# Kernel optimization log

Measured on AMD Instinct MI355X. Metric: run time of the kernel, lower is better.

## Reference

```python
import jax, jax.numpy as jnp
import numpy as np

N_NODES = 100_000
N_EDGES = 1_600_000
F_IN = 64
HID = 128
HEAD_H = 256
OUT = 32
N_GRAPHS = 512
NEG_SLOPE = 0.01  # torch.nn.LeakyReLU default


def _leaky(v):
    return jnp.where(v >= 0, v, NEG_SLOPE * v)


def _gine_layer(x, src, dst, edge_attr, We, be, Wn, bn, n_nodes):
    # GINEConv (eps=0): nn( x_i + sum_j relu(x_j + lin(edge_attr_ji)) )
    msg = jax.nn.relu(x[src] + edge_attr @ We + be)          # [E, in]
    agg = jax.ops.segment_sum(msg, dst, num_segments=n_nodes)  # [N, in]
    return (agg + x) @ Wn + bn                                # [N, hid]


def setup_inputs() -> dict:
    key = jax.random.key(0)
    ks = jax.random.split(key, 24)
    inp = {}
    inp["x"] = jax.random.normal(ks[0], (N_NODES, F_IN), dtype=jnp.float32)
    inp["edge_index"] = jax.random.randint(ks[1], (2, N_EDGES), 0, N_NODES, dtype=jnp.int32)
    inp["edge_attr"] = jax.random.normal(ks[2], (N_EDGES, 2), dtype=jnp.float32)
    inp["batch"] = jnp.sort(jax.random.randint(ks[3], (N_NODES,), 0, N_GRAPHS, dtype=jnp.int32))
    # GINE layers: edge lin (2 -> in) and nn Linear (in -> hid)
    dims = [F_IN, HID, HID]
    ki = 4
    for l, d_in in enumerate(dims):
        inp[f"We{l}"] = jax.random.normal(ks[ki], (2, d_in), dtype=jnp.float32) / np.sqrt(2.0); ki += 1
        inp[f"be{l}"] = jnp.zeros((d_in,), dtype=jnp.float32)
        inp[f"Wn{l}"] = jax.random.normal(ks[ki], (d_in, HID), dtype=jnp.float32) / np.sqrt(d_in); ki += 1
        inp[f"bn{l}"] = jnp.zeros((HID,), dtype=jnp.float32)
    # head MLP
    inp["Wh0"] = jax.random.normal(ks[ki], (HID, HEAD_H), dtype=jnp.float32) / np.sqrt(HID); ki += 1
    inp["bh0"] = jnp.zeros((HEAD_H,), dtype=jnp.float32)
    inp["Wh1"] = jax.random.normal(ks[ki], (HEAD_H, OUT), dtype=jnp.float32) / np.sqrt(HEAD_H); ki += 1
    inp["bh1"] = jnp.zeros((OUT,), dtype=jnp.float32)
    return inp


def reference(x, edge_index, edge_attr, batch,
              We0, be0, Wn0, bn0,
              We1, be1, Wn1, bn1,
              We2, be2, Wn2, bn2,
              Wh0, bh0, Wh1, bh1):
    src, dst = edge_index[0], edge_index[1]
    h = _leaky(_gine_layer(x, src, dst, edge_attr, We0, be0, Wn0, bn0, N_NODES))
    h = _leaky(_gine_layer(h, src, dst, edge_attr, We1, be1, Wn1, bn1, N_NODES))
    h = _leaky(_gine_layer(h, src, dst, edge_attr, We2, be2, Wn2, bn2, N_NODES))
    pooled = jax.ops.segment_sum(h, batch, num_segments=N_GRAPHS)  # [G, HID]
    h = _leaky(pooled @ Wh0 + bh0)
    return h @ Wh1 + bh1  # [G, OUT]
```

## Files before the change

### kernel.cpp

```cpp
#include <hip/hip_runtime.h>
#include <hip/hip_bf16.h>

#define N_NODES 100000
#define N_EDGES 1600000
#define F_IN 64
#define HID 128
#define HEAD_H 256
#define OUT_F 32
#define N_GRAPHS 512
#define NBK 98
#define BCHUNK 4096
#define NCHUNKS ((N_EDGES + BCHUNK - 1) / BCHUNK)

typedef float f2v __attribute__((ext_vector_type(2)));
typedef short bf16x8 __attribute__((ext_vector_type(8)));
typedef float f32x4 __attribute__((ext_vector_type(4)));

__device__ __forceinline__ float leaky(float v) {
    return v >= 0.f ? v : 0.01f * v;
}

__device__ __forceinline__ float bf2f(ushort u) {
    union { uint i; float f; } c; c.i = ((uint)u) << 16; return c.f;
}

__device__ __forceinline__ ushort f2bf(float f) {
    union { float f; uint i; } c; c.f = f;
    uint r = c.i + 0x7FFF + ((c.i >> 16) & 1);
    return (ushort)(r >> 16);
}

__global__ __launch_bounds__(256) void cast_kernel(const float* __restrict__ x,
                                                   ushort* __restrict__ xb, int n2) {
    int i = blockIdx.x * 256 + threadIdx.x;
    if (i < n2) {
        float2 v = ((const float2*)x)[i];
        uint u = (uint)f2bf(v.x) | ((uint)f2bf(v.y) << 16);
        ((uint*)xb)[i] = u;
    }
}

__global__ __launch_bounds__(256) void prep_wnT(const float* __restrict__ Wn0,
                                                const float* __restrict__ Wn1,
                                                const float* __restrict__ Wn2,
                                                ushort* __restrict__ w0T,
                                                ushort* __restrict__ w1T,
                                                ushort* __restrict__ w2T) {
    int id = blockIdx.x * 256 + threadIdx.x;
    if (id < 128 * 64) {
        int j = id / 64, k = id % 64;
        w0T[id] = f2bf(Wn0[k * 128 + j]);
    } else if (id < 128 * 64 + 128 * 128) {
        int t = id - 128 * 64; int j = t / 128, k = t % 128;
        w1T[t] = f2bf(Wn1[k * 128 + j]);
    } else if (id < 128 * 64 + 2 * 128 * 128) {
        int t = id - 128 * 64 - 128 * 128; int j = t / 128, k = t % 128;
        w2T[t] = f2bf(Wn2[k * 128 + j]);
    }
}


__global__ __launch_bounds__(256) void bucket_hist(const int* __restrict__ dst,
                                                   int* __restrict__ cnt98) {
    __shared__ int h[NBK];
    int tid = threadIdx.x;
    if (tid < NBK) h[tid] = 0;
    __syncthreads();
    int e0 = blockIdx.x * BCHUNK;
    int nn = N_EDGES - e0; if (nn > BCHUNK) nn = BCHUNK;
    for (int i = tid; i < nn; i += 256) {
        atomicAdd(&h[dst[e0 + i] >> 10], 1);
    }
    __syncthreads();
    if (tid < NBK && h[tid] > 0) atomicAdd(&cnt98[tid], h[tid]);
}

__global__ __launch_bounds__(128) void bucket_scan(const int* __restrict__ cnt98,
                                                   int* __restrict__ bbase,
                                                   int* __restrict__ bcur,
                                                   int* __restrict__ rowptr) {
    __shared__ int sd[128];
    int t = threadIdx.x;
    int v = (t < NBK) ? cnt98[t] : 0;
    sd[t] = v;
    __syncthreads();
    for (int off = 1; off < 128; off <<= 1) {
        int u = (t >= off) ? sd[t - off] : 0;
        __syncthreads();
        sd[t] += u;
        __syncthreads();
    }
    if (t < NBK) {
        int ex = sd[t] - v;
        bbase[t] = ex;
        bcur[t] = ex;
    }
    if (t == 0) {
        bbase[NBK] = N_EDGES;
        rowptr[N_NODES] = N_EDGES;
    }
}

__global__ __launch_bounds__(256) void bin_kernel(const int* __restrict__ src,
                                                  const int* __restrict__ dst,
                                                  const float2* __restrict__ ea,
                                                  int* __restrict__ bcur,
                                                  uint2* __restrict__ recs1) {
    __shared__ int hist[NBK], tmp[NBK], offs[NBK], cur[NBK], gbase[NBK];
    __shared__ uint2 stage[BCHUNK];
    __shared__ unsigned char sbid[BCHUNK];

    int tid = threadIdx.x;
    int e0 = blockIdx.x * BCHUNK;
    int nn = N_EDGES - e0; if (nn > BCHUNK) nn = BCHUNK;

    if (tid < NBK) hist[tid] = 0;
    __syncthreads();

    for (int i = tid; i < nn; i += 256) {
        atomicAdd(&hist[dst[e0 + i] >> 10], 1);
    }
    __syncthreads();

    if (tid < NBK) tmp[tid] = hist[tid];
    __syncthreads();
    for (int off = 1; off < NBK; off <<= 1) {
        int u = (tid < NBK && tid >= off) ? tmp[tid - off] : 0;
        __syncthreads();
        if (tid < NBK) tmp[tid] += u;
        __syncthreads();
    }
    if (tid < NBK) {
        int ex = tmp[tid] - hist[tid];
        offs[tid] = ex;
        cur[tid] = ex;
        gbase[tid] = (hist[tid] > 0) ? atomicAdd(&bcur[tid], hist[tid]) : 0;
    }
    __syncthreads();

    for (int i = tid; i < nn; i += 256) {
        int e = e0 + i;
        int d = dst[e];
        int b = d >> 10;
        int dloc = d & 1023;
        float2 a = ea[e];
        uint2 r;
        r.x = (uint)src[e] | ((uint)dloc << 22);
        r.y = (uint)f2bf(a.x) | ((uint)f2bf(a.y) << 16);
        int pos = atomicAdd(&cur[b], 1);
        stage[pos] = r;
        sbid[pos] = (unsigned char)b;
    }
    __syncthreads();

    for (int i = tid; i < nn; i += 256) {
        int b = sbid[i];
        recs1[gbase[b] + (i - offs[b])] = stage[i];
    }
}

__global__ __launch_bounds__(256) void order_kernel(const uint2* __restrict__ recs1,
                                                    const int* __restrict__ bbase,
                                                    int* __restrict__ rowptr,
                                                    uint2* __restrict__ recs2) {
    __shared__ int h[1024];
    __shared__ int ssum[256];
    int b = blockIdx.x;
    int tid = threadIdx.x;
    int base = bbase[b];
    int end = bbase[b + 1];

    for (int i = tid; i < 1024; i += 256) h[i] = 0;
    __syncthreads();

    for (int t = base + tid; t < end; t += 256) {
        atomicAdd(&h[recs1[t].x >> 22], 1);
    }
    __syncthreads();

    int i4 = tid * 4;
    int a0 = h[i4], a1 = h[i4 + 1], a2 = h[i4 + 2], a3 = h[i4 + 3];
    int s = a0 + a1 + a2 + a3;
    ssum[tid] = s;
    __syncthreads();
    for (int off = 1; off < 256; off <<= 1) {
        int u = (tid >= off) ? ssum[tid - off] : 0;
        __syncthreads();
        ssum[tid] += u;
        __syncthreads();
    }
    int pre = base + ssum[tid] - s;
    int c0 = pre, c1 = pre + a0, c2 = c1 + a1, c3 = c2 + a2;
    h[i4] = c0; h[i4 + 1] = c1; h[i4 + 2] = c2; h[i4 + 3] = c3;

    int n = (b << 10) + i4;
    if (n + 4 <= N_NODES) {
        *(int4*)(rowptr + n) = make_int4(c0, c1, c2, c3);
    } else {
        if (n + 0 < N_NODES) rowptr[n + 0] = c0;
        if (n + 1 < N_NODES) rowptr[n + 1] = c1;
        if (n + 2 < N_NODES) rowptr[n + 2] = c2;
        if (n + 3 < N_NODES) rowptr[n + 3] = c3;
    }
    __syncthreads();

    for (int t = base + tid; t < end; t += 256) {
        uint2 r = recs1[t];
        int pos = atomicAdd(&h[r.x >> 22], 1);
        recs2[pos] = make_uint2(r.x & 0x3FFFFFu, r.y);
    }
}


template <int D>
__global__ __launch_bounds__(256) void gine_gather(const ushort* __restrict__ xb,
                                                   const uint2* __restrict__ recs,
                                                   const int* __restrict__ rowptr,
                                                   const float* __restrict__ We,
                                                   const float* __restrict__ be,
                                                   ushort* __restrict__ tb) {
    int node = (blockIdx.x * 256 + (int)threadIdx.x) >> 6;
    int lane = threadIdx.x & 63;
    if (node >= N_NODES) return;

    int rs = __builtin_amdgcn_readfirstlane(rowptr[node]);
    int re = __builtin_amdgcn_readfirstlane(rowptr[node + 1]);

    if constexpr (D == 128) {
        int j = lane * 2;
        f2v w0v = {We[j], We[j + 1]};
        f2v w1v = {We[128 + j], We[128 + j + 1]};
        f2v bbv = {be[j], be[j + 1]};
        f2v accv = {0.f, 0.f};
        const f2v zero = {0.f, 0.f};

        auto proc = [&](uint2 r, uint u) {
            float ax = bf2f((ushort)(r.y & 0xFFFF));
            float ay = bf2f((ushort)(r.y >> 16));
            union { uint i; float f; } lo, hi;
            lo.i = u << 16;
            hi.i = u & 0xFFFF0000u;
            f2v xv = {lo.f, hi.f};
            f2v m = xv + bbv;
            m = ay * w1v + m;
            m = ax * w0v + m;
            m = __builtin_elementwise_max(m, zero);
            accv += m;
        };

        int t = rs;
        for (; t + 7 < re; t += 8) {
            uint2 r0 = recs[t];
            uint2 r1 = recs[t + 1];
            uint2 r2 = recs[t + 2];
            uint2 r3 = recs[t + 3];
            uint2 r4 = recs[t + 4];
            uint2 r5 = recs[t + 5];
            uint2 r6 = recs[t + 6];
            uint2 r7 = recs[t + 7];
            uint u0 = *(const uint*)(xb + (size_t)r0.x * 128 + j);
            uint u1 = *(const uint*)(xb + (size_t)r1.x * 128 + j);
            uint u2 = *(const uint*)(xb + (size_t)r2.x * 128 + j);
            uint u3 = *(const uint*)(xb + (size_t)r3.x * 128 + j);
            uint u4 = *(const uint*)(xb + (size_t)r4.x * 128 + j);
            uint u5 = *(const uint*)(xb + (size_t)r5.x * 128 + j);
            uint u6 = *(const uint*)(xb + (size_t)r6.x * 128 + j);
            uint u7 = *(const uint*)(xb + (size_t)r7.x * 128 + j);
            proc(r0, u0); proc(r1, u1); proc(r2, u2); proc(r3, u3);
            proc(r4, u4); proc(r5, u5); proc(r6, u6); proc(r7, u7);
        }
        for (; t + 3 < re; t += 4) {
            uint2 r0 = recs[t];
            uint2 r1 = recs[t + 1];
            uint2 r2 = recs[t + 2];
            uint2 r3 = recs[t + 3];
            uint u0 = *(const uint*)(xb + (size_t)r0.x * 128 + j);
            uint u1 = *(const uint*)(xb + (size_t)r1.x * 128 + j);
            uint u2 = *(const uint*)(xb + (size_t)r2.x * 128 + j);
            uint u3 = *(const uint*)(xb + (size_t)r3.x * 128 + j);
            proc(r0, u0); proc(r1, u1); proc(r2, u2); proc(r3, u3);
        }
        for (; t < re; t++) {
            uint2 r0 = recs[t];
            uint u0 = *(const uint*)(xb + (size_t)r0.x * 128 + j);
            proc(r0, u0);
        }

        {
            uint u = *(const uint*)(xb + (size_t)node * 128 + j);
            union { uint i; float f; } lo, hi;
            lo.i = u << 16;
            hi.i = u & 0xFFFF0000u;
            f2v xv = {lo.f, hi.f};
            accv += xv;
        }
        uint up = (uint)f2bf(accv.x) | ((uint)f2bf(accv.y) << 16);
        ((uint*)tb)[(size_t)node * 64 + lane] = up;
    } else {
        float w0 = We[lane], w1 = We[64 + lane], bb = be[lane];
        float acc = 0.f;

        auto proc = [&](uint2 r, ushort u) {
            float ax = bf2f((ushort)(r.y & 0xFFFF));
            float ay = bf2f((ushort)(r.y >> 16));
            float m = bf2f(u) + bb;
            m = ay * w1 + m;
            m = ax * w0 + m;
            acc += fmaxf(m, 0.f);
        };

        int t = rs;
        for (; t + 7 < re; t += 8) {
            uint2 r0 = recs[t];
            uint2 r1 = recs[t + 1];
            uint2 r2 = recs[t + 2];
            uint2 r3 = recs[t + 3];
            uint2 r4 = recs[t + 4];
            uint2 r5 = recs[t + 5];
            uint2 r6 = recs[t + 6];
            uint2 r7 = recs[t + 7];
            ushort u0 = xb[(size_t)r0.x * 64 + lane];
            ushort u1 = xb[(size_t)r1.x * 64 + lane];
            ushort u2 = xb[(size_t)r2.x * 64 + lane];
            ushort u3 = xb[(size_t)r3.x * 64 + lane];
            ushort u4 = xb[(size_t)r4.x * 64 + lane];
            ushort u5 = xb[(size_t)r5.x * 64 + lane];
            ushort u6 = xb[(size_t)r6.x * 64 + lane];
            ushort u7 = xb[(size_t)r7.x * 64 + lane];
            proc(r0, u0); proc(r1, u1); proc(r2, u2); proc(r3, u3);
            proc(r4, u4); proc(r5, u5); proc(r6, u6); proc(r7, u7);
        }
        for (; t + 3 < re; t += 4) {
            uint2 r0 = recs[t];
            uint2 r1 = recs[t + 1];
            uint2 r2 = recs[t + 2];
            uint2 r3 = recs[t + 3];
            ushort u0 = xb[(size_t)r0.x * 64 + lane];
            ushort u1 = xb[(size_t)r1.x * 64 + lane];
            ushort u2 = xb[(size_t)r2.x * 64 + lane];
            ushort u3 = xb[(size_t)r3.x * 64 + lane];
            proc(r0, u0); proc(r1, u1); proc(r2, u2); proc(r3, u3);
        }
        for (; t < re; t++) {
            uint2 r0 = recs[t];
            ushort u0 = xb[(size_t)r0.x * 64 + lane];
            proc(r0, u0);
        }
        acc += bf2f(xb[(size_t)node * 64 + lane]);
        tb[(size_t)node * 64 + lane] = f2bf(acc);
    }
}


template <int K>
__global__ __launch_bounds__(256) void gine_transform_mfma(const ushort* __restrict__ tb,
                                                           const ushort* __restrict__ wnT,
                                                           const float* __restrict__ bn,
                                                           ushort* __restrict__ hb) {
    int wave = threadIdx.x >> 6;
    int lane = threadIdx.x & 63;
    int m0 = blockIdx.x * 64 + wave * 16;
    int l15 = lane & 15;
    int kgrp = (lane >> 4) * 8;

    const ushort* aptr = tb + (size_t)(m0 + l15) * K + kgrp;

    f32x4 acc[8];
#pragma unroll
    for (int nt = 0; nt < 8; nt++) {
        float b = bn[nt * 16 + l15];
        acc[nt] = {b, b, b, b};
    }

#pragma unroll
    for (int kk = 0; kk < K / 32; kk++) {
        bf16x8 a = *(const bf16x8*)(aptr + kk * 32);
#pragma unroll
        for (int nt = 0; nt < 8; nt++) {
            bf16x8 bfrag = *(const bf16x8*)(wnT + (size_t)(nt * 16 + l15) * K + kk * 32 + kgrp);
            acc[nt] = __builtin_amdgcn_mfma_f32_16x16x32_bf16(a, bfrag, acc[nt], 0, 0, 0);
        }
    }

    int rbase = m0 + (lane >> 4) * 4;
#pragma unroll
    for (int nt = 0; nt < 8; nt++) {
#pragma unroll
        for (int r = 0; r < 4; r++) {
            int nd = rbase + r;
            if (nd < N_NODES)
                hb[(size_t)nd * HID + nt * 16 + l15] = f2bf(leaky(acc[nt][r]));
        }
    }
}

#define POOL_NPW 64
__global__ __launch_bounds__(256) void pool_kernel(const ushort* __restrict__ h,
                                                   const int* __restrict__ batch,
                                                   float* __restrict__ pooled) {
    int wid = (blockIdx.x * 256 + (int)threadIdx.x) >> 6;
    int lane = threadIdx.x & 63;
    int n0 = wid * POOL_NPW;
    if (n0 >= N_NODES) return;
    int n1 = n0 + POOL_NPW; if (n1 > N_NODES) n1 = N_NODES;

    int j = lane * 2;
    f2v acc = {0.f, 0.f};
    int g = __builtin_amdgcn_readfirstlane(batch[n0]);
    for (int i = n0; i < n1; i++) {
        int bg = __builtin_amdgcn_readfirstlane(batch[i]);
        if (bg != g) {
            atomicAdd(&pooled[g * HID + j], acc.x);
            atomicAdd(&pooled[g * HID + j + 1], acc.y);
            acc.x = 0.f; acc.y = 0.f;
            g = bg;
        }
        uint u = *(const uint*)(h + (size_t)i * HID + j);
        union { uint i; float f; } lo, hi;
        lo.i = u << 16;
        hi.i = u & 0xFFFF0000u;
        acc.x += lo.f;
        acc.y += hi.f;
    }
    atomicAdd(&pooled[g * HID + j], acc.x);
    atomicAdd(&pooled[g * HID + j + 1], acc.y);
}


__global__ __launch_bounds__(256) void head_kernel(const float* __restrict__ pooled,
                                                   const float* __restrict__ Wh0,
                                                   const float* __restrict__ bh0,
                                                   const float* __restrict__ Wh1,
                                                   const float* __restrict__ bh1,
                                                   float* __restrict__ out) {
    __shared__ float p[HID];
    __shared__ float hid[HEAD_H];
    int g = blockIdx.x;
    int t = threadIdx.x;
    if (t < HID) p[t] = pooled[g * HID + t];
    __syncthreads();
    float acc = bh0[t];
    for (int k = 0; k < HID; k++) acc += p[k] * Wh0[k * HEAD_H + t];
    hid[t] = leaky(acc);
    __syncthreads();
    if (t < OUT_F) {
        float o = bh1[t];
        for (int k = 0; k < HEAD_H; k++) o += hid[k] * Wh1[k * OUT_F + t];
        out[g * OUT_F + t] = o;
    }
}

extern "C" void kernel_launch(void* const* d_in, const int* in_sizes, int n_in,
                              void* d_out, int out_size, void* d_ws, size_t ws_size,
                              hipStream_t stream) {
    const float* x     = (const float*)d_in[0];
    const int*   ei    = (const int*)d_in[1];
    const float* ea    = (const float*)d_in[2];
    const int*   batch = (const int*)d_in[3];
    const float* We0 = (const float*)d_in[4];
    const float* be0 = (const float*)d_in[5];
    const float* Wn0 = (const float*)d_in[6];
    const float* bn0 = (const float*)d_in[7];
    const float* We1 = (const float*)d_in[8];
    const float* be1 = (const float*)d_in[9];
    const float* Wn1 = (const float*)d_in[10];
    const float* bn1 = (const float*)d_in[11];
    const float* We2 = (const float*)d_in[12];
    const float* be2 = (const float*)d_in[13];
    const float* Wn2 = (const float*)d_in[14];
    const float* bn2 = (const float*)d_in[15];
    const float* Wh0 = (const float*)d_in[16];
    const float* bh0 = (const float*)d_in[17];
    const float* Wh1 = (const float*)d_in[18];
    const float* bh1 = (const float*)d_in[19];

    const int* src = ei;
    const int* dst = ei + N_EDGES;

    char* ws = (char*)d_ws;
    size_t o = 0;
    uint2*  recs1 = (uint2*)(ws + o); o += (size_t)N_EDGES * 8;
    uint2*  recs2 = (uint2*)(ws + o); o += (size_t)N_EDGES * 8;
    ushort* xb0  = (ushort*)(ws + o); o += (size_t)N_NODES * 64 * 2;
    ushort* tbuf = (ushort*)(ws + o); o += (size_t)N_NODES * 128 * 2;
    ushort* hbuf = (ushort*)(ws + o); o += (size_t)N_NODES * 128 * 2;
    int*    rowptr = (int*)(ws + o);  o += 400128;
    int*    cnt98  = (int*)(ws + o);  o += 4096;
    int*    bbase  = (int*)(ws + o);  o += 4096;
    int*    bcur   = (int*)(ws + o);  o += 4096;
    ushort* wnT0 = (ushort*)(ws + o); o += 128 * 64 * 2;
    ushort* wnT1 = (ushort*)(ws + o); o += 128 * 128 * 2;
    ushort* wnT2 = (ushort*)(ws + o); o += 128 * 128 * 2;
    float*  pooled = (float*)(ws + o); o += (size_t)N_GRAPHS * HID * 4;

    cast_kernel<<<(N_NODES * F_IN / 2 + 255) / 256, 256, 0, stream>>>(x, xb0, N_NODES * F_IN / 2);
    prep_wnT<<<160, 256, 0, stream>>>(Wn0, Wn1, Wn2, wnT0, wnT1, wnT2);

    hipMemsetAsync(cnt98, 0, NBK * sizeof(int), stream);
    bucket_hist<<<NCHUNKS, 256, 0, stream>>>(dst, cnt98);
    bucket_scan<<<1, 128, 0, stream>>>(cnt98, bbase, bcur, rowptr);
    bin_kernel<<<NCHUNKS, 256, 0, stream>>>(src, dst, (const float2*)ea, bcur, recs1);
    order_kernel<<<NBK, 256, 0, stream>>>(recs1, bbase, rowptr, recs2);

    const int GATHER_BLOCKS = (N_NODES * 64 + 255) / 256;
    const int TRANS_BLOCKS  = (N_NODES + 63) / 64;

    gine_gather<64><<<GATHER_BLOCKS, 256, 0, stream>>>(xb0, recs2, rowptr, We0, be0, tbuf);
    gine_transform_mfma<64><<<TRANS_BLOCKS, 256, 0, stream>>>(tbuf, wnT0, bn0, hbuf);

    gine_gather<128><<<GATHER_BLOCKS, 256, 0, stream>>>(hbuf, recs2, rowptr, We1, be1, tbuf);
    gine_transform_mfma<128><<<TRANS_BLOCKS, 256, 0, stream>>>(tbuf, wnT1, bn1, hbuf);

    gine_gather<128><<<GATHER_BLOCKS, 256, 0, stream>>>(hbuf, recs2, rowptr, We2, be2, tbuf);
    gine_transform_mfma<128><<<TRANS_BLOCKS, 256, 0, stream>>>(tbuf, wnT2, bn2, hbuf);

    hipMemsetAsync(pooled, 0, (size_t)N_GRAPHS * HID * sizeof(float), stream);
    pool_kernel<<<(N_NODES / POOL_NPW + 3) / 4, 256, 0, stream>>>(hbuf, batch, pooled);
    head_kernel<<<N_GRAPHS, 256, 0, stream>>>(pooled, Wh0, bh0, Wh1, bh1, (float*)d_out);
}
```

Baseline: 393.8 us.

## Fuse edge gather and MFMA node transform into one kernel per GINE layer

Replaces the separate gather and MFMA transform kernels with one fused kernel per layer. Each 1024-thread block handles 16 nodes: its 16 waves split the block's edge range evenly and accumulate into swizzled LDS with shared-memory atomics. The first 8 waves then add the self features and run the 16x16x32 bf16 MFMA straight from LDS. This removes the bf16 intermediate buffer round trip and two launches, and evens out per-wave edge load. In exchange it adds LDS atomic traffic, block-wide barriers, and only half the waves working in the matmul phase.

```diff
diff --git a/kernel.cpp b/kernel.cpp
--- a/kernel.cpp
+++ b/kernel.cpp
@@ -207,34 +207,58 @@
     for (int t = base + tid; t < end; t += 256) {
         uint2 r = recs1[t];
         int pos = atomicAdd(&h[r.x >> 22], 1);
-        recs2[pos] = make_uint2(r.x & 0x3FFFFFu, r.y);
-    }
-}
-
-
-template <int D>
-__global__ __launch_bounds__(256) void gine_gather(const ushort* __restrict__ xb,
+        recs2[pos] = r;
+    }
+}
+
+
+template <int K>
+__global__ __launch_bounds__(1024) void gine_fused(const ushort* __restrict__ xb,
                                                    const uint2* __restrict__ recs,
                                                    const int* __restrict__ rowptr,
                                                    const float* __restrict__ We,
                                                    const float* __restrict__ be,
-                                                   ushort* __restrict__ tb) {
-    int node = (blockIdx.x * 256 + (int)threadIdx.x) >> 6;
-    int lane = threadIdx.x & 63;
-    if (node >= N_NODES) return;
-
-    int rs = __builtin_amdgcn_readfirstlane(rowptr[node]);
-    int re = __builtin_amdgcn_readfirstlane(rowptr[node + 1]);
-
-    if constexpr (D == 128) {
+                                                   const ushort* __restrict__ wnT,
+                                                   const float* __restrict__ bn,
+                                                   ushort* __restrict__ hb) {
+    __shared__ float acc_s[16 * K];
+    int tid = threadIdx.x;
+    int wave = __builtin_amdgcn_readfirstlane(tid >> 6);
+    int lane = tid & 63;
+    int n0 = blockIdx.x * 16;
+
+    for (int i = tid; i < 16 * K; i += 1024) acc_s[i] = 0.f;
+
+    int base = __builtin_amdgcn_readfirstlane(rowptr[n0]);
+    int end  = __builtin_amdgcn_readfirstlane(rowptr[n0 + 16]);
+    __syncthreads();
+
+    int E = end - base;
+    int per = (E + 15) >> 4;
+    int t0 = base + wave * per;
+    int t1 = t0 + per; if (t1 > end) t1 = end;
+
+    if constexpr (K == 128) {
         int j = lane * 2;
         f2v w0v = {We[j], We[j + 1]};
         f2v w1v = {We[128 + j], We[128 + j + 1]};
         f2v bbv = {be[j], be[j + 1]};
         f2v accv = {0.f, 0.f};
         const f2v zero = {0.f, 0.f};
-
+        int cur = -1;
+
+        auto flush = [&]() {
+            int idx = (cur * 128 + j) ^ ((cur & 7) << 2);
+            atomicAdd(&acc_s[idx], accv.x);
+            atomicAdd(&acc_s[idx + 1], accv.y);
+        };
         auto proc = [&](uint2 r, uint u) {
+            int local = (int)(r.x >> 22) & 15;
+            if (local != cur) {
+                if (cur >= 0) flush();
+                cur = local;
+                accv = zero;
+            }
             float ax = bf2f((ushort)(r.y & 0xFFFF));
             float ay = bf2f((ushort)(r.y >> 16));
             union { uint i; float f; } lo, hi;
@@ -248,59 +272,40 @@
             accv += m;
         };
 
-        int t = rs;
-        for (; t + 7 < re; t += 8) {
+        int t = t0;
+        for (; t + 3 < t1; t += 4) {
             uint2 r0 = recs[t];
             uint2 r1 = recs[t + 1];
             uint2 r2 = recs[t + 2];
             uint2 r3 = recs[t + 3];
-            uint2 r4 = recs[t + 4];
-            uint2 r5 = recs[t + 5];
-            uint2 r6 = recs[t + 6];
-            uint2 r7 = recs[t + 7];
-            uint u0 = *(const uint*)(xb + (size_t)r0.x * 128 + j);
-            uint u1 = *(const uint*)(xb + (size_t)r1.x * 128 + j);
-            uint u2 = *(const uint*)(xb + (size_t)r2.x * 128 + j);
-            uint u3 = *(const uint*)(xb + (size_t)r3.x * 128 + j);
-            uint u4 = *(const uint*)(xb + (size_t)r4.x * 128 + j);
-            uint u5 = *(const uint*)(xb + (size_t)r5.x * 128 + j);
-            uint u6 = *(const uint*)(xb + (size_t)r6.x * 128 + j);
-            uint u7 = *(const uint*)(xb + (size_t)r7.x * 128 + j);
+            uint u0 = *(const uint*)(xb + (size_t)(r0.x & 0x3FFFFFu) * 128 + j);
+            uint u1 = *(const uint*)(xb + (size_t)(r1.x & 0x3FFFFFu) * 128 + j);
+            uint u2 = *(const uint*)(xb + (size_t)(r2.x & 0x3FFFFFu) * 128 + j);
+            uint u3 = *(const uint*)(xb + (size_t)(r3.x & 0x3FFFFFu) * 128 + j);
             proc(r0, u0); proc(r1, u1); proc(r2, u2); proc(r3, u3);
-            proc(r4, u4); proc(r5, u5); proc(r6, u6); proc(r7, u7);
-        }
-        for (; t + 3 < re; t += 4) {
+        }
+        for (; t < t1; t++) {
             uint2 r0 = recs[t];
-            uint2 r1 = recs[t + 1];
-            uint2 r2 = recs[t + 2];
-            uint2 r3 = recs[t + 3];
-            uint u0 = *(const uint*)(xb + (size_t)r0.x * 128 + j);
-            uint u1 = *(const uint*)(xb + (size_t)r1.x * 128 + j);
-            uint u2 = *(const uint*)(xb + (size_t)r2.x * 128 + j);
-            uint u3 = *(const uint*)(xb + (size_t)r3.x * 128 + j);
-            proc(r0, u0); proc(r1, u1); proc(r2, u2); proc(r3, u3);
-        }
-        for (; t < re; t++) {
-            uint2 r0 = recs[t];
-            uint u0 = *(const uint*)(xb + (size_t)r0.x * 128 + j);
+            uint u0 = *(const uint*)(xb + (size_t)(r0.x & 0x3FFFFFu) * 128 + j);
             proc(r0, u0);
         }
-
-        {
-            uint u = *(const uint*)(xb + (size_t)node * 128 + j);
-            union { uint i; float f; } lo, hi;
-            lo.i = u << 16;
-            hi.i = u & 0xFFFF0000u;
-            f2v xv = {lo.f, hi.f};
-            accv += xv;
-        }
-        uint up = (uint)f2bf(accv.x) | ((uint)f2bf(accv.y) << 16);
-        ((uint*)tb)[(size_t)node * 64 + lane] = up;
+        if (cur >= 0) flush();
     } else {
         float w0 = We[lane], w1 = We[64 + lane], bb = be[lane];
         float acc = 0.f;
-
+        int cur = -1;
+
+        auto flush = [&]() {
+            int idx = (cur * 64 + lane) ^ ((cur & 7) << 2);
+            atomicAdd(&acc_s[idx], acc);
+        };
         auto proc = [&](uint2 r, ushort u) {
+            int local = (int)(r.x >> 22) & 15;
+            if (local != cur) {
+                if (cur >= 0) flush();
+                cur = local;
+                acc = 0.f;
+            }
             float ax = bf2f((ushort)(r.y & 0xFFFF));
             float ay = bf2f((ushort)(r.y >> 16));
             float m = bf2f(u) + bb;
@@ -309,87 +314,58 @@
             acc += fmaxf(m, 0.f);
         };
 
-        int t = rs;
-        for (; t + 7 < re; t += 8) {
+        int t = t0;
+        for (; t + 3 < t1; t += 4) {
             uint2 r0 = recs[t];
             uint2 r1 = recs[t + 1];
             uint2 r2 = recs[t + 2];
             uint2 r3 = recs[t + 3];
-            uint2 r4 = recs[t + 4];
-            uint2 r5 = recs[t + 5];
-            uint2 r6 = recs[t + 6];
-            uint2 r7 = recs[t + 7];
-            ushort u0 = xb[(size_t)r0.x * 64 + lane];
-            ushort u1 = xb[(size_t)r1.x * 64 + lane];
-            ushort u2 = xb[(size_t)r2.x * 64 + lane];
-            ushort u3 = xb[(size_t)r3.x * 64 + lane];
-            ushort u4 = xb[(size_t)r4.x * 64 + lane];
-            ushort u5 = xb[(size_t)r5.x * 64 + lane];
-            ushort u6 = xb[(size_t)r6.x * 64 + lane];
-            ushort u7 = xb[(size_t)r7.x * 64 + lane];
+            ushort u0 = xb[(size_t)(r0.x & 0x3FFFFFu) * 64 + lane];
+            ushort u1 = xb[(size_t)(r1.x & 0x3FFFFFu) * 64 + lane];
+            ushort u2 = xb[(size_t)(r2.x & 0x3FFFFFu) * 64 + lane];
+            ushort u3 = xb[(size_t)(r3.x & 0x3FFFFFu) * 64 + lane];
             proc(r0, u0); proc(r1, u1); proc(r2, u2); proc(r3, u3);
-            proc(r4, u4); proc(r5, u5); proc(r6, u6); proc(r7, u7);
-        }
-        for (; t + 3 < re; t += 4) {
+        }
+        for (; t < t1; t++) {
             uint2 r0 = recs[t];
-            uint2 r1 = recs[t + 1];
-            uint2 r2 = recs[t + 2];
-            uint2 r3 = recs[t + 3];
-            ushort u0 = xb[(size_t)r0.x * 64 + lane];
-            ushort u1 = xb[(size_t)r1.x * 64 + lane];
-            ushort u2 = xb[(size_t)r2.x * 64 + lane];
-            ushort u3 = xb[(size_t)r3.x * 64 + lane];
-            proc(r0, u0); proc(r1, u1); proc(r2, u2); proc(r3, u3);
-        }
-        for (; t < re; t++) {
-            uint2 r0 = recs[t];
-            ushort u0 = xb[(size_t)r0.x * 64 + lane];
+            ushort u0 = xb[(size_t)(r0.x & 0x3FFFFFu) * 64 + lane];
             proc(r0, u0);
         }
-        acc += bf2f(xb[(size_t)node * 64 + lane]);
-        tb[(size_t)node * 64 + lane] = f2bf(acc);
-    }
-}
-
-
-template <int K>
-__global__ __launch_bounds__(256) void gine_transform_mfma(const ushort* __restrict__ tb,
-                                                           const ushort* __restrict__ wnT,
-                                                           const float* __restrict__ bn,
-                                                           ushort* __restrict__ hb) {
-    int wave = threadIdx.x >> 6;
-    int lane = threadIdx.x & 63;
-    int m0 = blockIdx.x * 64 + wave * 16;
-    int l15 = lane & 15;
-    int kgrp = (lane >> 4) * 8;
-
-    const ushort* aptr = tb + (size_t)(m0 + l15) * K + kgrp;
-
-    f32x4 acc[8];
+        if (cur >= 0) flush();
+    }
+    __syncthreads();
+
+    if (wave < 8) {
+        int nt = wave;
+        int l15 = lane & 15;
+        int kgrp = (lane >> 4) * 8;
+        int row = l15;
+        int sw = (row & 7) << 2;
+        float b = bn[nt * 16 + l15];
+        f32x4 acc = {b, b, b, b};
+
 #pragma unroll
-    for (int nt = 0; nt < 8; nt++) {
-        float b = bn[nt * 16 + l15];
-        acc[nt] = {b, b, b, b};
-    }
-
+        for (int kk = 0; kk < K / 32; kk++) {
+            int k0 = kk * 32 + kgrp;
+            int i0 = (row * K + k0) ^ sw;
+            int i1 = (row * K + k0 + 4) ^ sw;
+            f32x4 p0 = *(const f32x4*)&acc_s[i0];
+            f32x4 p1 = *(const f32x4*)&acc_s[i1];
+            bf16x8 xr = *(const bf16x8*)(xb + (size_t)(n0 + row) * K + k0);
+            bf16x8 a;
 #pragma unroll
-    for (int kk = 0; kk < K / 32; kk++) {
-        bf16x8 a = *(const bf16x8*)(aptr + kk * 32);
-#pragma unroll
-        for (int nt = 0; nt < 8; nt++) {
-            bf16x8 bfrag = *(const bf16x8*)(wnT + (size_t)(nt * 16 + l15) * K + kk * 32 + kgrp);
-            acc[nt] = __builtin_amdgcn_mfma_f32_16x16x32_bf16(a, bfrag, acc[nt], 0, 0, 0);
-        }
-    }
-
-    int rbase = m0 + (lane >> 4) * 4;
-#pragma unroll
-    for (int nt = 0; nt < 8; nt++) {
+            for (int e = 0; e < 4; e++) {
+                a[e]     = (short)f2bf(p0[e] + bf2f((ushort)xr[e]));
+                a[e + 4] = (short)f2bf(p1[e] + bf2f((ushort)xr[e + 4]));
+            }
+            bf16x8 bfrag = *(const bf16x8*)(wnT + (size_t)(nt * 16 + l15) * K + k0);
+            acc = __builtin_amdgcn_mfma_f32_16x16x32_bf16(a, bfrag, acc, 0, 0, 0);
+        }
+
+        int rbase = n0 + (lane >> 4) * 4;
 #pragma unroll
         for (int r = 0; r < 4; r++) {
-            int nd = rbase + r;
-            if (nd < N_NODES)
-                hb[(size_t)nd * HID + nt * 16 + l15] = f2bf(leaky(acc[nt][r]));
+            hb[(size_t)(rbase + r) * HID + nt * 16 + l15] = f2bf(leaky(acc[r]));
         }
     }
 }
@@ -482,8 +458,8 @@
     uint2*  recs1 = (uint2*)(ws + o); o += (size_t)N_EDGES * 8;
     uint2*  recs2 = (uint2*)(ws + o); o += (size_t)N_EDGES * 8;
     ushort* xb0  = (ushort*)(ws + o); o += (size_t)N_NODES * 64 * 2;
-    ushort* tbuf = (ushort*)(ws + o); o += (size_t)N_NODES * 128 * 2;
-    ushort* hbuf = (ushort*)(ws + o); o += (size_t)N_NODES * 128 * 2;
+    ushort* hbufA = (ushort*)(ws + o); o += (size_t)N_NODES * 128 * 2;
+    ushort* hbufB = (ushort*)(ws + o); o += (size_t)N_NODES * 128 * 2;
     int*    rowptr = (int*)(ws + o);  o += 400128;
     int*    cnt98  = (int*)(ws + o);  o += 4096;
     int*    bbase  = (int*)(ws + o);  o += 4096;
@@ -502,19 +478,13 @@
     bin_kernel<<<NCHUNKS, 256, 0, stream>>>(src, dst, (const float2*)ea, bcur, recs1);
     order_kernel<<<NBK, 256, 0, stream>>>(recs1, bbase, rowptr, recs2);
 
-    const int GATHER_BLOCKS = (N_NODES * 64 + 255) / 256;
-    const int TRANS_BLOCKS  = (N_NODES + 63) / 64;
-
-    gine_gather<64><<<GATHER_BLOCKS, 256, 0, stream>>>(xb0, recs2, rowptr, We0, be0, tbuf);
-    gine_transform_mfma<64><<<TRANS_BLOCKS, 256, 0, stream>>>(tbuf, wnT0, bn0, hbuf);
-
-    gine_gather<128><<<GATHER_BLOCKS, 256, 0, stream>>>(hbuf, recs2, rowptr, We1, be1, tbuf);
-    gine_transform_mfma<128><<<TRANS_BLOCKS, 256, 0, stream>>>(tbuf, wnT1, bn1, hbuf);
-
-    gine_gather<128><<<GATHER_BLOCKS, 256, 0, stream>>>(hbuf, recs2, rowptr, We2, be2, tbuf);
-    gine_transform_mfma<128><<<TRANS_BLOCKS, 256, 0, stream>>>(tbuf, wnT2, bn2, hbuf);
+    const int FUSED_BLOCKS = N_NODES / 16;
+
+    gine_fused<64><<<FUSED_BLOCKS, 1024, 0, stream>>>(xb0, recs2, rowptr, We0, be0, wnT0, bn0, hbufA);
+    gine_fused<128><<<FUSED_BLOCKS, 1024, 0, stream>>>(hbufA, recs2, rowptr, We1, be1, wnT1, bn1, hbufB);
+    gine_fused<128><<<FUSED_BLOCKS, 1024, 0, stream>>>(hbufB, recs2, rowptr, We2, be2, wnT2, bn2, hbufA);
 
     hipMemsetAsync(pooled, 0, (size_t)N_GRAPHS * HID * sizeof(float), stream);
-    pool_kernel<<<(N_NODES / POOL_NPW + 3) / 4, 256, 0, stream>>>(hbuf, batch, pooled);
+    pool_kernel<<<(N_NODES / POOL_NPW + 3) / 4, 256, 0, stream>>>(hbufA, batch, pooled);
     head_kernel<<<N_GRAPHS, 256, 0, stream>>>(pooled, Wh0, bh0, Wh1, bh1, (float*)d_out);
 }
```

Result: slower. 570.5 us (+44.9%).

## Fuse GINE gather and MFMA transform into one kernel per layer

Applied to the files above, without the earlier changes.

Merges the per-layer edge gather-aggregate and the bf16 MFMA node transform into a single kernel. Each block of four waves aggregates 16 nodes into a swizzled fp32 LDS tile, adds the self features, then runs the 16x128 MFMA with each wave computing two output column tiles. This drops the intermediate tbuf round trip and one launch per layer, and ping-pongs between two h buffers. In exchange each block covers only 16 rows, so the Wn fragments are reloaded from global/L2 per block, and each wave walks four nodes in sequence, which can increase load imbalance.

```diff
diff --git a/kernel.cpp b/kernel.cpp
--- a/kernel.cpp
+++ b/kernel.cpp
@@ -212,184 +212,188 @@
 }
 
 
-template <int D>
-__global__ __launch_bounds__(256) void gine_gather(const ushort* __restrict__ xb,
-                                                   const uint2* __restrict__ recs,
-                                                   const int* __restrict__ rowptr,
-                                                   const float* __restrict__ We,
-                                                   const float* __restrict__ be,
-                                                   ushort* __restrict__ tb) {
-    int node = (blockIdx.x * 256 + (int)threadIdx.x) >> 6;
-    int lane = threadIdx.x & 63;
-    if (node >= N_NODES) return;
-
-    int rs = __builtin_amdgcn_readfirstlane(rowptr[node]);
-    int re = __builtin_amdgcn_readfirstlane(rowptr[node + 1]);
-
-    if constexpr (D == 128) {
+template <int K>
+__global__ __launch_bounds__(256) void gine_fused(const ushort* __restrict__ xb,
+                                                  const uint2* __restrict__ recs,
+                                                  const int* __restrict__ rowptr,
+                                                  const float* __restrict__ We,
+                                                  const float* __restrict__ be,
+                                                  const ushort* __restrict__ wnT,
+                                                  const float* __restrict__ bn,
+                                                  ushort* __restrict__ hb) {
+    __shared__ float tile[16 * K];
+    int tid = threadIdx.x;
+    int wave = tid >> 6;
+    int lane = tid & 63;
+    int n0 = blockIdx.x * 16;
+
+    if constexpr (K == 128) {
         int j = lane * 2;
         f2v w0v = {We[j], We[j + 1]};
         f2v w1v = {We[128 + j], We[128 + j + 1]};
         f2v bbv = {be[j], be[j + 1]};
-        f2v accv = {0.f, 0.f};
         const f2v zero = {0.f, 0.f};
 
-        auto proc = [&](uint2 r, uint u) {
-            float ax = bf2f((ushort)(r.y & 0xFFFF));
-            float ay = bf2f((ushort)(r.y >> 16));
-            union { uint i; float f; } lo, hi;
-            lo.i = u << 16;
-            hi.i = u & 0xFFFF0000u;
-            f2v xv = {lo.f, hi.f};
-            f2v m = xv + bbv;
-            m = ay * w1v + m;
-            m = ax * w0v + m;
-            m = __builtin_elementwise_max(m, zero);
-            accv += m;
-        };
-
-        int t = rs;
-        for (; t + 7 < re; t += 8) {
-            uint2 r0 = recs[t];
-            uint2 r1 = recs[t + 1];
-            uint2 r2 = recs[t + 2];
-            uint2 r3 = recs[t + 3];
-            uint2 r4 = recs[t + 4];
-            uint2 r5 = recs[t + 5];
-            uint2 r6 = recs[t + 6];
-            uint2 r7 = recs[t + 7];
-            uint u0 = *(const uint*)(xb + (size_t)r0.x * 128 + j);
-            uint u1 = *(const uint*)(xb + (size_t)r1.x * 128 + j);
-            uint u2 = *(const uint*)(xb + (size_t)r2.x * 128 + j);
-            uint u3 = *(const uint*)(xb + (size_t)r3.x * 128 + j);
-            uint u4 = *(const uint*)(xb + (size_t)r4.x * 128 + j);
-            uint u5 = *(const uint*)(xb + (size_t)r5.x * 128 + j);
-            uint u6 = *(const uint*)(xb + (size_t)r6.x * 128 + j);
-            uint u7 = *(const uint*)(xb + (size_t)r7.x * 128 + j);
-            proc(r0, u0); proc(r1, u1); proc(r2, u2); proc(r3, u3);
-            proc(r4, u4); proc(r5, u5); proc(r6, u6); proc(r7, u7);
+        for (int q = 0; q < 4; q++) {
+            int node = n0 + wave * 4 + q;
+            int rs = __builtin_amdgcn_readfirstlane(rowptr[node]);
+            int re = __builtin_amdgcn_readfirstlane(rowptr[node + 1]);
+            f2v accv = {0.f, 0.f};
+
+            auto proc = [&](uint2 r, uint u) {
+                float ax = bf2f((ushort)(r.y & 0xFFFF));
+                float ay = bf2f((ushort)(r.y >> 16));
+                union { uint i; float f; } lo, hi;
+                lo.i = u << 16;
+                hi.i = u & 0xFFFF0000u;
+                f2v xv = {lo.f, hi.f};
+                f2v m = xv + bbv;
+                m = ay * w1v + m;
+                m = ax * w0v + m;
+                m = __builtin_elementwise_max(m, zero);
+                accv += m;
+            };
+
+            int t = rs;
+            for (; t + 7 < re; t += 8) {
+                uint2 r0 = recs[t];
+                uint2 r1 = recs[t + 1];
+                uint2 r2 = recs[t + 2];
+                uint2 r3 = recs[t + 3];
+                uint2 r4 = recs[t + 4];
+                uint2 r5 = recs[t + 5];
+                uint2 r6 = recs[t + 6];
+                uint2 r7 = recs[t + 7];
+                uint u0 = *(const uint*)(xb + (size_t)r0.x * 128 + j);
+                uint u1 = *(const uint*)(xb + (size_t)r1.x * 128 + j);
+                uint u2 = *(const uint*)(xb + (size_t)r2.x * 128 + j);
+                uint u3 = *(const uint*)(xb + (size_t)r3.x * 128 + j);
+                uint u4 = *(const uint*)(xb + (size_t)r4.x * 128 + j);
+                uint u5 = *(const uint*)(xb + (size_t)r5.x * 128 + j);
+                uint u6 = *(const uint*)(xb + (size_t)r6.x * 128 + j);
+                uint u7 = *(const uint*)(xb + (size_t)r7.x * 128 + j);
+                proc(r0, u0); proc(r1, u1); proc(r2, u2); proc(r3, u3);
+                proc(r4, u4); proc(r5, u5); proc(r6, u6); proc(r7, u7);
+            }
+            for (; t + 3 < re; t += 4) {
+                uint2 r0 = recs[t];
+                uint2 r1 = recs[t + 1];
+                uint2 r2 = recs[t + 2];
+                uint2 r3 = recs[t + 3];
+                uint u0 = *(const uint*)(xb + (size_t)r0.x * 128 + j);
+                uint u1 = *(const uint*)(xb + (size_t)r1.x * 128 + j);
+                uint u2 = *(const uint*)(xb + (size_t)r2.x * 128 + j);
+                uint u3 = *(const uint*)(xb + (size_t)r3.x * 128 + j);
+                proc(r0, u0); proc(r1, u1); proc(r2, u2); proc(r3, u3);
+            }
+            for (; t < re; t++) {
+                uint2 r0 = recs[t];
+                uint u0 = *(const uint*)(xb + (size_t)r0.x * 128 + j);
+                proc(r0, u0);
+            }
+
+            int row = node & 15;
+            int idx = (row * 128 + j) ^ ((row & 7) << 2);
+            *(f2v*)&tile[idx] = accv;
         }
-        for (; t + 3 < re; t += 4) {
-            uint2 r0 = recs[t];
-            uint2 r1 = recs[t + 1];
-            uint2 r2 = recs[t + 2];
-            uint2 r3 = recs[t + 3];
-            uint u0 = *(const uint*)(xb + (size_t)r0.x * 128 + j);
-            uint u1 = *(const uint*)(xb + (size_t)r1.x * 128 + j);
-            uint u2 = *(const uint*)(xb + (size_t)r2.x * 128 + j);
-            uint u3 = *(const uint*)(xb + (size_t)r3.x * 128 + j);
-            proc(r0, u0); proc(r1, u1); proc(r2, u2); proc(r3, u3);
-        }
-        for (; t < re; t++) {
-            uint2 r0 = recs[t];
-            uint u0 = *(const uint*)(xb + (size_t)r0.x * 128 + j);
-            proc(r0, u0);
-        }
-
-        {
-            uint u = *(const uint*)(xb + (size_t)node * 128 + j);
-            union { uint i; float f; } lo, hi;
-            lo.i = u << 16;
-            hi.i = u & 0xFFFF0000u;
-            f2v xv = {lo.f, hi.f};
-            accv += xv;
-        }
-        uint up = (uint)f2bf(accv.x) | ((uint)f2bf(accv.y) << 16);
-        ((uint*)tb)[(size_t)node * 64 + lane] = up;
     } else {
         float w0 = We[lane], w1 = We[64 + lane], bb = be[lane];
-        float acc = 0.f;
-
-        auto proc = [&](uint2 r, ushort u) {
-            float ax = bf2f((ushort)(r.y & 0xFFFF));
-            float ay = bf2f((ushort)(r.y >> 16));
-            float m = bf2f(u) + bb;
-            m = ay * w1 + m;
-            m = ax * w0 + m;
-            acc += fmaxf(m, 0.f);
-        };
-
-        int t = rs;
-        for (; t + 7 < re; t += 8) {
-            uint2 r0 = recs[t];
-            uint2 r1 = recs[t + 1];
-            uint2 r2 = recs[t + 2];
-            uint2 r3 = recs[t + 3];
-            uint2 r4 = recs[t + 4];
-            uint2 r5 = recs[t + 5];
-            uint2 r6 = recs[t + 6];
-            uint2 r7 = recs[t + 7];
-            ushort u0 = xb[(size_t)r0.x * 64 + lane];
-            ushort u1 = xb[(size_t)r1.x * 64 + lane];
-            ushort u2 = xb[(size_t)r2.x * 64 + lane];
-            ushort u3 = xb[(size_t)r3.x * 64 + lane];
-            ushort u4 = xb[(size_t)r4.x * 64 + lane];
-            ushort u5 = xb[(size_t)r5.x * 64 + lane];
-            ushort u6 = xb[(size_t)r6.x * 64 + lane];
-            ushort u7 = xb[(size_t)r7.x * 64 + lane];
-            proc(r0, u0); proc(r1, u1); proc(r2, u2); proc(r3, u3);
-            proc(r4, u4); proc(r5, u5); proc(r6, u6); proc(r7, u7);
+
+        for (int q = 0; q < 4; q++) {
+            int node = n0 + wave * 4 + q;
+            int rs = __builtin_amdgcn_readfirstlane(rowptr[node]);
+            int re = __builtin_amdgcn_readfirstlane(rowptr[node + 1]);
+            float acc = 0.f;
+
+            auto proc = [&](uint2 r, ushort u) {
+                float ax = bf2f((ushort)(r.y & 0xFFFF));
+                float ay = bf2f((ushort)(r.y >> 16));
+                float m = bf2f(u) + bb;
+                m = ay * w1 + m;
+                m = ax * w0 + m;
+                acc += fmaxf(m, 0.f);
+            };
+
+            int t = rs;
+            for (; t + 7 < re; t += 8) {
+                uint2 r0 = recs[t];
+                uint2 r1 = recs[t + 1];
+                uint2 r2 = recs[t + 2];
+                uint2 r3 = recs[t + 3];
+                uint2 r4 = recs[t + 4];
+                uint2 r5 = recs[t + 5];
+                uint2 r6 = recs[t + 6];
+                uint2 r7 = recs[t + 7];
+                ushort u0 = xb[(size_t)r0.x * 64 + lane];
+                ushort u1 = xb[(size_t)r1.x * 64 + lane];
+                ushort u2 = xb[(size_t)r2.x * 64 + lane];
+                ushort u3 = xb[(size_t)r3.x * 64 + lane];
+                ushort u4 = xb[(size_t)r4.x * 64 + lane];
+                ushort u5 = xb[(size_t)r5.x * 64 + lane];
+                ushort u6 = xb[(size_t)r6.x * 64 + lane];
+                ushort u7 = xb[(size_t)r7.x * 64 + lane];
+                proc(r0, u0); proc(r1, u1); proc(r2, u2); proc(r3, u3);
+                proc(r4, u4); proc(r5, u5); proc(r6, u6); proc(r7, u7);
+            }
+            for (; t + 3 < re; t += 4) {
+                uint2 r0 = recs[t];
+                uint2 r1 = recs[t + 1];
+                uint2 r2 = recs[t + 2];
+                uint2 r3 = recs[t + 3];
+                ushort u0 = xb[(size_t)r0.x * 64 + lane];
+                ushort u1 = xb[(size_t)r1.x * 64 + lane];
+                ushort u2 = xb[(size_t)r2.x * 64 + lane];
+                ushort u3 = xb[(size_t)r3.x * 64 + lane];
+                proc(r0, u0); proc(r1, u1); proc(r2, u2); proc(r3, u3);
+            }
+            for (; t < re; t++) {
+                uint2 r0 = recs[t];
+                ushort u0 = xb[(size_t)r0.x * 64 + lane];
+                proc(r0, u0);
+            }
+
+            int row = node & 15;
+            int idx = (row * 64 + lane) ^ ((row & 7) << 2);
+            tile[idx] = acc;
         }
-        for (; t + 3 < re; t += 4) {
-            uint2 r0 = recs[t];
-            uint2 r1 = recs[t + 1];
-            uint2 r2 = recs[t + 2];
-            uint2 r3 = recs[t + 3];
-            ushort u0 = xb[(size_t)r0.x * 64 + lane];
-            ushort u1 = xb[(size_t)r1.x * 64 + lane];
-            ushort u2 = xb[(size_t)r2.x * 64 + lane];
-            ushort u3 = xb[(size_t)r3.x * 64 + lane];
-            proc(r0, u0); proc(r1, u1); proc(r2, u2); proc(r3, u3);
+    }
+    __syncthreads();
+
+    {
+        int l15 = lane & 15;
+        int kgrp = (lane >> 4) * 8;
+        int row = l15;
+        int sw = (row & 7) << 2;
+        int nt0 = wave * 2;
+        int nt1 = nt0 + 1;
+        float b0 = bn[nt0 * 16 + l15];
+        float b1 = bn[nt1 * 16 + l15];
+        f32x4 acc0 = {b0, b0, b0, b0};
+        f32x4 acc1 = {b1, b1, b1, b1};
+
+#pragma unroll
+        for (int kk = 0; kk < K / 32; kk++) {
+            int k0 = kk * 32 + kgrp;
+            f32x4 p0 = *(const f32x4*)&tile[(row * K + k0) ^ sw];
+            f32x4 p1 = *(const f32x4*)&tile[(row * K + k0 + 4) ^ sw];
+            bf16x8 xr = *(const bf16x8*)(xb + (size_t)(n0 + row) * K + k0);
+            bf16x8 a;
+#pragma unroll
+            for (int e = 0; e < 4; e++) {
+                a[e]     = (short)f2bf(p0[e] + bf2f((ushort)xr[e]));
+                a[e + 4] = (short)f2bf(p1[e] + bf2f((ushort)xr[e + 4]));
+            }
+            bf16x8 bf0 = *(const bf16x8*)(wnT + (size_t)(nt0 * 16 + l15) * K + k0);
+            bf16x8 bf1 = *(const bf16x8*)(wnT + (size_t)(nt1 * 16 + l15) * K + k0);
+            acc0 = __builtin_amdgcn_mfma_f32_16x16x32_bf16(a, bf0, acc0, 0, 0, 0);
+            acc1 = __builtin_amdgcn_mfma_f32_16x16x32_bf16(a, bf1, acc1, 0, 0, 0);
         }
-        for (; t < re; t++) {
-            uint2 r0 = recs[t];
-            ushort u0 = xb[(size_t)r0.x * 64 + lane];
-            proc(r0, u0);
-        }
-        acc += bf2f(xb[(size_t)node * 64 + lane]);
-        tb[(size_t)node * 64 + lane] = f2bf(acc);
-    }
-}
-
-
-template <int K>
-__global__ __launch_bounds__(256) void gine_transform_mfma(const ushort* __restrict__ tb,
-                                                           const ushort* __restrict__ wnT,
-                                                           const float* __restrict__ bn,
-                                                           ushort* __restrict__ hb) {
-    int wave = threadIdx.x >> 6;
-    int lane = threadIdx.x & 63;
-    int m0 = blockIdx.x * 64 + wave * 16;
-    int l15 = lane & 15;
-    int kgrp = (lane >> 4) * 8;
-
-    const ushort* aptr = tb + (size_t)(m0 + l15) * K + kgrp;
-
-    f32x4 acc[8];
-#pragma unroll
-    for (int nt = 0; nt < 8; nt++) {
-        float b = bn[nt * 16 + l15];
-        acc[nt] = {b, b, b, b};
-    }
-
-#pragma unroll
-    for (int kk = 0; kk < K / 32; kk++) {
-        bf16x8 a = *(const bf16x8*)(aptr + kk * 32);
-#pragma unroll
-        for (int nt = 0; nt < 8; nt++) {
-            bf16x8 bfrag = *(const bf16x8*)(wnT + (size_t)(nt * 16 + l15) * K + kk * 32 + kgrp);
-            acc[nt] = __builtin_amdgcn_mfma_f32_16x16x32_bf16(a, bfrag, acc[nt], 0, 0, 0);
-        }
-    }
-
-    int rbase = m0 + (lane >> 4) * 4;
-#pragma unroll
-    for (int nt = 0; nt < 8; nt++) {
+
+        int rbase = n0 + (lane >> 4) * 4;
 #pragma unroll
         for (int r = 0; r < 4; r++) {
-            int nd = rbase + r;
-            if (nd < N_NODES)
-                hb[(size_t)nd * HID + nt * 16 + l15] = f2bf(leaky(acc[nt][r]));
+            hb[(size_t)(rbase + r) * HID + nt0 * 16 + l15] = f2bf(leaky(acc0[r]));
+            hb[(size_t)(rbase + r) * HID + nt1 * 16 + l15] = f2bf(leaky(acc1[r]));
         }
     }
 }
@@ -482,8 +486,8 @@
     uint2*  recs1 = (uint2*)(ws + o); o += (size_t)N_EDGES * 8;
     uint2*  recs2 = (uint2*)(ws + o); o += (size_t)N_EDGES * 8;
     ushort* xb0  = (ushort*)(ws + o); o += (size_t)N_NODES * 64 * 2;
-    ushort* tbuf = (ushort*)(ws + o); o += (size_t)N_NODES * 128 * 2;
-    ushort* hbuf = (ushort*)(ws + o); o += (size_t)N_NODES * 128 * 2;
+    ushort* hbufA = (ushort*)(ws + o); o += (size_t)N_NODES * 128 * 2;
+    ushort* hbufB = (ushort*)(ws + o); o += (size_t)N_NODES * 128 * 2;
     int*    rowptr = (int*)(ws + o);  o += 400128;
     int*    cnt98  = (int*)(ws + o);  o += 4096;
     int*    bbase  = (int*)(ws + o);  o += 4096;
@@ -502,19 +506,13 @@
     bin_kernel<<<NCHUNKS, 256, 0, stream>>>(src, dst, (const float2*)ea, bcur, recs1);
     order_kernel<<<NBK, 256, 0, stream>>>(recs1, bbase, rowptr, recs2);
 
-    const int GATHER_BLOCKS = (N_NODES * 64 + 255) / 256;
-    const int TRANS_BLOCKS  = (N_NODES + 63) / 64;
-
-    gine_gather<64><<<GATHER_BLOCKS, 256, 0, stream>>>(xb0, recs2, rowptr, We0, be0, tbuf);
-    gine_transform_mfma<64><<<TRANS_BLOCKS, 256, 0, stream>>>(tbuf, wnT0, bn0, hbuf);
-
-    gine_gather<128><<<GATHER_BLOCKS, 256, 0, stream>>>(hbuf, recs2, rowptr, We1, be1, tbuf);
-    gine_transform_mfma<128><<<TRANS_BLOCKS, 256, 0, stream>>>(tbuf, wnT1, bn1, hbuf);
-
-    gine_gather<128><<<GATHER_BLOCKS, 256, 0, stream>>>(hbuf, recs2, rowptr, We2, be2, tbuf);
-    gine_transform_mfma<128><<<TRANS_BLOCKS, 256, 0, stream>>>(tbuf, wnT2, bn2, hbuf);
+    const int FUSED_BLOCKS = N_NODES / 16;
+
+    gine_fused<64><<<FUSED_BLOCKS, 256, 0, stream>>>(xb0, recs2, rowptr, We0, be0, wnT0, bn0, hbufA);
+    gine_fused<128><<<FUSED_BLOCKS, 256, 0, stream>>>(hbufA, recs2, rowptr, We1, be1, wnT1, bn1, hbufB);
+    gine_fused<128><<<FUSED_BLOCKS, 256, 0, stream>>>(hbufB, recs2, rowptr, We2, be2, wnT2, bn2, hbufA);
 
     hipMemsetAsync(pooled, 0, (size_t)N_GRAPHS * HID * sizeof(float), stream);
-    pool_kernel<<<(N_NODES / POOL_NPW + 3) / 4, 256, 0, stream>>>(hbuf, batch, pooled);
+    pool_kernel<<<(N_NODES / POOL_NPW + 3) / 4, 256, 0, stream>>>(hbufA, batch, pooled);
     head_kernel<<<N_GRAPHS, 256, 0, stream>>>(pooled, Wh0, bh0, Wh1, bh1, (float*)d_out);
 }
```

New measurement: 367.5 us. 1.07x faster.
